# Performance work log

Measured on AMD Instinct MI355X. Metric: run time of the kernel, lower is better.

## Reference

```python
import jax, jax.numpy as jnp
import numpy as np

NUM_HEADS = 16
PREFIX = 64  # always-refreshed prefix tokens


def setup_inputs() -> dict:
    key = jax.random.key(0)
    ks = jax.random.split(key, 6)
    B, N, C = 64, 320, 1024
    H, D = NUM_HEADS, C // NUM_HEADS
    MAX_KV = 1024
    x = jax.random.normal(ks[0], (B, N, C), dtype=jnp.float32)
    # pre-existing cache contents (old cached K/V at positions 64:64+cur_kv_len matter)
    k_cache = jax.random.normal(ks[1], (B, H, MAX_KV, D), dtype=jnp.float32)
    v_cache = jax.random.normal(ks[2], (B, H, MAX_KV, D), dtype=jnp.float32)
    w_qkv = jax.random.normal(ks[3], (C, 3 * C), dtype=jnp.float32) * 0.02
    w_proj = jax.random.normal(ks[4], (C, C), dtype=jnp.float32) * 0.02
    b_proj = jnp.zeros((C,), dtype=jnp.float32)
    cur_kv_len = 256
    return {"x": x, "k_cache": k_cache, "v_cache": v_cache,
            "w_qkv": w_qkv, "w_proj": w_proj, "b_proj": b_proj,
            "cur_kv_len": cur_kv_len}


def reference(x, k_cache, v_cache, w_qkv, w_proj, b_proj, cur_kv_len):
    # Lazy-MAR incremental path (lazy_mar=True, is_force_fresh=False).
    B, N, C = x.shape
    H = NUM_HEADS
    D = C // H
    scale = D ** -0.5
    app = N - PREFIX  # number of new tokens appended to the cache

    # qkv projection (qkv_bias=False), split into q/k/v of shape [B, H, N, D]
    qkv = (x @ w_qkv).reshape(B, N, 3, H, D).transpose(2, 0, 3, 1, 4)
    q, k, v = qkv[0], qkv[1], qkv[2]  # qk_norm=False -> identity

    # in-place cache writes: refresh prefix [0:64], append new tokens at 64+cur_kv_len
    k_cache = k_cache.at[:, :, :PREFIX, :].set(k[:, :, :PREFIX, :])
    k_cache = k_cache.at[:, :, PREFIX + cur_kv_len:PREFIX + cur_kv_len + app, :].set(k[:, :, PREFIX:, :])
    v_cache = v_cache.at[:, :, :PREFIX, :].set(v[:, :, :PREFIX, :])
    v_cache = v_cache.at[:, :, PREFIX + cur_kv_len:PREFIX + cur_kv_len + app, :].set(v[:, :, PREFIX:, :])

    avail = cur_kv_len + app + PREFIX  # = cur_kv_len + N
    kk = k_cache[:, :, :avail, :]  # [B, H, avail, D]
    vv = v_cache[:, :, :avail, :]

    # manual QK^T -> softmax -> AV (attn_drop = 0)
    attn = jnp.einsum('bhnd,bhmd->bhnm', q * scale, kk)
    attn = jax.nn.softmax(attn, axis=-1)
    out = jnp.einsum('bhnm,bhmd->bhnd', attn, vv)  # [B, H, N, D]

    out = out.transpose(0, 2, 1, 3).reshape(B, N, C)
    return out @ w_proj + b_proj
```

## Files before the change

### kernel.cpp

```cpp
#include <hip/hip_runtime.h>
#include <hip/hip_bf16.h>

typedef unsigned int u32;
typedef unsigned short u16;
typedef __attribute__((ext_vector_type(4))) float f32x4;
typedef __attribute__((ext_vector_type(8))) short bf16x8;

static __device__ __forceinline__ u16 f2b(float f) {
  u32 u = __float_as_uint(f);
  u = (u + 0x7fffu + ((u >> 16) & 1u)) >> 16;
  return (u16)u;
}
static __device__ __forceinline__ u32 pk2(float a, float b) {
  return (u32)f2b(a) | ((u32)f2b(b) << 16);
}

#define AS1(p) ((__attribute__((address_space(1))) u32*)(p))
#define AS3(p) ((__attribute__((address_space(3))) u32*)(p))

union Frag  { bf16x8 v; u32 w[4]; };
union Pack8 { u32 w[8]; int4 q[2]; };

__global__ __launch_bounds__(256)
void cast_bf16(const float* __restrict__ in, u16* __restrict__ out)
{
  const size_t i = ((size_t)blockIdx.x * 256 + threadIdx.x) * 8;
  float4 a = *(const float4*)(in + i);
  float4 b = *(const float4*)(in + i + 4);
  Pack8 pb;
  pb.w[0] = pk2(a.x, a.y); pb.w[1] = pk2(a.z, a.w);
  pb.w[2] = pk2(b.x, b.y); pb.w[3] = pk2(b.z, b.w);
  *(int4*)(out + i) = pb.q[0];
}

__global__ __launch_bounds__(256)
void transpose_cvt(const float* __restrict__ in, u16* __restrict__ out,
                   int R, int C, int scale_rows)
{
  __shared__ float tile[64][65];
  const int tx = threadIdx.x & 63, ty = threadIdx.x >> 6;
  const int c0 = blockIdx.x * 64, r0 = blockIdx.y * 64;
#pragma unroll
  for (int i = 0; i < 64; i += 4)
    tile[ty + i][tx] = in[(size_t)(r0 + ty + i) * C + c0 + tx];
  __syncthreads();
#pragma unroll
  for (int i = 0; i < 64; i += 4) {
    int oc = c0 + ty + i;
    float v = tile[tx][ty + i];
    if (oc < scale_rows) v *= 0.125f;
    out[(size_t)oc * R + r0 + tx] = f2b(v);
  }
}

template<int MODE>
__global__ __launch_bounds__(256)
void gemm_bt(const u16* __restrict__ Ap, const u16* __restrict__ Bt, int NBX,
             u16* __restrict__ o_q, u16* __restrict__ o_k, u16* __restrict__ o_vt,
             const float* __restrict__ bias, float* __restrict__ outp)
{
  constexpr int K = 1024;
  constexpr int NT = 32;
  __shared__ __align__(16) u16 Al[2][128 * 32];
  __shared__ __align__(16) u16 Bl[2][128 * 32];

  const int tid = threadIdx.x;
  const int l = tid & 63, wid = tid >> 6;
  const int lr = l & 15, lg = l >> 4;
  const int wm = wid >> 1, wn = wid & 1;

  const int nwg = gridDim.x;
  const int qq = nwg >> 3;
  const int nb = (blockIdx.x & 7) * qq + (blockIdx.x >> 3);
  const int bx = nb % NBX, by = nb / NBX;

  f32x4 acc[4][4] = {};

  auto stageG = [&](int buf, int t) {
    const int k0 = t * 32;
#pragma unroll
    for (int it = 0; it < 2; ++it) {
      int row = it * 64 + (tid >> 2);
      int kb = (tid & 3) ^ (row & 3);
      const u16* g = Bt + (size_t)(bx * 128 + row) * K + k0 + kb * 8;
      __builtin_amdgcn_global_load_lds(AS1(g), AS3(&Bl[buf][0] + it * 2048 + tid * 8), 16, 0, 0);
    }
#pragma unroll
    for (int it = 0; it < 2; ++it) {
      int row = it * 64 + (tid >> 2);
      int kb = (tid & 3) ^ (row & 3);
      const u16* g = Ap + (size_t)(by * 128 + row) * K + k0 + kb * 8;
      __builtin_amdgcn_global_load_lds(AS1(g), AS3(&Al[buf][0] + it * 2048 + tid * 8), 16, 0, 0);
    }
  };

  stageG(0, 0);
  __syncthreads();

  for (int t = 0; t < NT; ++t) {
    const int cur = t & 1;
    if (t + 1 < NT) stageG(cur ^ 1, t + 1);
    bf16x8 af[4], bfr[4];
#pragma unroll
    for (int mt = 0; mt < 4; ++mt) {
      int row = wm * 64 + mt * 16 + lr;
      af[mt] = *(const bf16x8*)((const char*)&Al[cur][0] + row * 64 +
                                ((lg * 16) ^ ((row & 3) << 4)));
    }
#pragma unroll
    for (int nt = 0; nt < 4; ++nt) {
      int row = wn * 64 + nt * 16 + lr;
      bfr[nt] = *(const bf16x8*)((const char*)&Bl[cur][0] + row * 64 +
                                 ((lg * 16) ^ ((row & 3) << 4)));
    }
#pragma unroll
    for (int mt = 0; mt < 4; ++mt)
#pragma unroll
      for (int nt = 0; nt < 4; ++nt)
        acc[mt][nt] = __builtin_amdgcn_mfma_f32_16x16x32_bf16(af[mt], bfr[nt], acc[mt][nt], 0, 0, 0);
    __syncthreads();
  }

  const int col0 = bx * 128 + wn * 64;
  if (MODE == 0) {
    const int s = col0 >> 10;
    const int h = (col0 & 1023) >> 6;
#pragma unroll
    for (int mt = 0; mt < 4; ++mt) {
      int row0 = by * 128 + wm * 64 + mt * 16 + lg * 4;
      int b = row0 / 320;
      int n0 = row0 - b * 320;
      size_t bh = (size_t)(b * 16 + h);
#pragma unroll
      for (int nt = 0; nt < 4; ++nt) {
        int d = nt * 16 + lr;
        if (s == 2) {
          ushort4 p4 = make_ushort4(f2b(acc[mt][nt][0]), f2b(acc[mt][nt][1]),
                                    f2b(acc[mt][nt][2]), f2b(acc[mt][nt][3]));
          *(ushort4*)(o_vt + (bh * 64 + d) * 320 + n0) = p4;
        } else {
          u16* dst = (s == 0) ? o_q : o_k;
#pragma unroll
          for (int j = 0; j < 4; ++j)
            dst[(bh * 320 + n0 + j) * 64 + d] = f2b(acc[mt][nt][j]);
        }
      }
    }
  } else {
#pragma unroll
    for (int nt = 0; nt < 4; ++nt) {
      int col = col0 + nt * 16 + lr;
      float bv = bias[col];
#pragma unroll
      for (int mt = 0; mt < 4; ++mt)
#pragma unroll
        for (int j = 0; j < 4; ++j) {
          int row = by * 128 + wm * 64 + mt * 16 + lg * 4 + j;
          outp[(size_t)row * 1024 + col] = acc[mt][nt][j] + bv;
        }
    }
  }
}

__global__ __launch_bounds__(256)
void attn_fused(const u16* __restrict__ q_bf, const u16* __restrict__ k_new,
                const u16* __restrict__ v_new_t,
                const float* __restrict__ k_cache, const float* __restrict__ v_cache,
                u16* __restrict__ attn_out)
{
  __shared__ __align__(16) u16 Kl[64 * 64];
  __shared__ __align__(16) u16 Vl[64 * 64];
  const int qt = blockIdx.x;
  const int bh = blockIdx.y;
  const int b = bh >> 4, h = bh & 15;
  const int tid = threadIdx.x;
  const int w = tid >> 6, l = tid & 63;
  const int lr = l & 15, lg = l >> 4;

  const int qrow = qt * 64 + w * 16 + lr;
  const u16* qp = q_bf + ((size_t)bh * 320 + qrow) * 64;
  const bf16x8 qf0 = *(const bf16x8*)(qp + lg * 8);
  const bf16x8 qf1 = *(const bf16x8*)(qp + 32 + lg * 8);

  f32x4 O[4] = {};
  float m = -1e30f, lsum = 0.f;

  for (int t = 0; t < 9; ++t) {
    __syncthreads();
    if (t == 0 || t >= 5) {
      const int n0 = (t == 0) ? 0 : t * 64 - 256;
#pragma unroll
      for (int it = 0; it < 2; ++it) {
        int slot = tid + it * 256;
        int row = slot >> 3, c = slot & 7;
        int4 v = *(const int4*)(k_new + ((size_t)bh * 320 + n0 + row) * 64 + c * 8);
        *(int4*)((char*)Kl + row * 128 + ((c * 16) ^ ((row & 7) << 4))) = v;
      }
#pragma unroll
      for (int it = 0; it < 2; ++it) {
        int slot = tid + it * 256;
        int row = slot >> 3, c = slot & 7;
        int4 v = *(const int4*)(v_new_t + ((size_t)bh * 64 + row) * 320 + n0 + c * 8);
        *(int4*)((char*)Vl + row * 128 + ((c * 16) ^ ((row & 7) << 4))) = v;
      }
    } else {
      const int pos0 = t * 64;
      {
        int r = tid >> 2, d0 = (tid & 3) * 16;
        const float* src = k_cache + ((size_t)bh * 1024 + pos0 + r) * 64 + d0;
        Pack8 pb;
#pragma unroll
        for (int i = 0; i < 4; ++i) {
          float4 f = *(const float4*)(src + i * 4);
          pb.w[i * 2] = pk2(f.x, f.y); pb.w[i * 2 + 1] = pk2(f.z, f.w);
        }
        char* base = (char*)Kl + r * 128;
        int c0 = d0 >> 3;
        *(int4*)(base + ((c0 * 16) ^ ((r & 7) << 4)))       = pb.q[0];
        *(int4*)(base + (((c0 + 1) * 16) ^ ((r & 7) << 4))) = pb.q[1];
      }
#pragma unroll
      for (int it = 0; it < 4; ++it) {
        int r = (tid >> 4) + it * 16;
        int d0 = (tid & 15) * 4;
        float4 f = *(const float4*)(v_cache + ((size_t)bh * 1024 + pos0 + r) * 64 + d0);
        float fv[4] = {f.x, f.y, f.z, f.w};
#pragma unroll
        for (int i = 0; i < 4; ++i) {
          int d = d0 + i;
          *(u16*)((char*)Vl + ((d * 128 + r * 2) ^ ((d & 7) << 4))) = f2b(fv[i]);
        }
      }
    }
    __syncthreads();

    f32x4 s[4];
#pragma unroll
    for (int nt = 0; nt < 4; ++nt) {
      f32x4 a = {};
      int kv = nt * 16 + lr;
      const char* kb = (const char*)Kl + kv * 128;
      bf16x8 k0 = *(const bf16x8*)(kb + ((lg * 16) ^ ((kv & 7) << 4)));
      bf16x8 k1 = *(const bf16x8*)(kb + ((64 + lg * 16) ^ ((kv & 7) << 4)));
      a = __builtin_amdgcn_mfma_f32_16x16x32_bf16(k0, qf0, a, 0, 0, 0);
      a = __builtin_amdgcn_mfma_f32_16x16x32_bf16(k1, qf1, a, 0, 0, 0);
      s[nt] = a;
    }

    float tmax = s[0][0];
#pragma unroll
    for (int nt = 0; nt < 4; ++nt)
#pragma unroll
      for (int j = 0; j < 4; ++j) tmax = fmaxf(tmax, s[nt][j]);
    tmax = fmaxf(tmax, __shfl_xor(tmax, 16));
    tmax = fmaxf(tmax, __shfl_xor(tmax, 32));
    const float mnew = fmaxf(m, tmax);
    const float corr = __expf(m - mnew);
    float psum = 0.f;
    u32 plo[4], phi[4];
#pragma unroll
    for (int nt = 0; nt < 4; ++nt) {
      float p0 = __expf(s[nt][0] - mnew);
      float p1 = __expf(s[nt][1] - mnew);
      float p2 = __expf(s[nt][2] - mnew);
      float p3 = __expf(s[nt][3] - mnew);
      psum += (p0 + p1) + (p2 + p3);
      plo[nt] = pk2(p0, p1);
      phi[nt] = pk2(p2, p3);
    }
    psum += __shfl_xor(psum, 16);
    psum += __shfl_xor(psum, 32);
    lsum = lsum * corr + psum;
    m = mnew;

    float c_[4];
#pragma unroll
    for (int j = 0; j < 4; ++j) c_[j] = __shfl(corr, lg * 4 + j);
#pragma unroll
    for (int dt = 0; dt < 4; ++dt)
#pragma unroll
      for (int j = 0; j < 4; ++j) O[dt][j] *= c_[j];

    const int srcA = (2 * (lg & 1)) * 16 + lr;
    const int srcB = srcA + 16;
    const int hi = lg >> 1;
#pragma unroll
    for (int p = 0; p < 2; ++p) {
      Frag pa;
      u32 a0 = (u32)__shfl((int)plo[2 * p], srcA), a1 = (u32)__shfl((int)plo[2 * p + 1], srcA);
      u32 b0 = (u32)__shfl((int)phi[2 * p], srcA), b1 = (u32)__shfl((int)phi[2 * p + 1], srcA);
      u32 a2 = (u32)__shfl((int)plo[2 * p], srcB), a3 = (u32)__shfl((int)plo[2 * p + 1], srcB);
      u32 b2 = (u32)__shfl((int)phi[2 * p], srcB), b3 = (u32)__shfl((int)phi[2 * p + 1], srcB);
      pa.w[0] = hi ? a1 : a0;
      pa.w[1] = hi ? b1 : b0;
      pa.w[2] = hi ? a3 : a2;
      pa.w[3] = hi ? b3 : b2;
#pragma unroll
      for (int dt = 0; dt < 4; ++dt) {
        int d = dt * 16 + lr;
        bf16x8 vf = *(const bf16x8*)((const char*)Vl + (size_t)d * 128 +
                                     ((p * 64 + lg * 16) ^ ((d & 7) << 4)));
        O[dt] = __builtin_amdgcn_mfma_f32_16x16x32_bf16(pa.v, vf, O[dt], 0, 0, 0);
      }
    }
  }

  float inv[4];
#pragma unroll
  for (int j = 0; j < 4; ++j) inv[j] = 1.f / __shfl(lsum, lg * 4 + j);
#pragma unroll
  for (int dt = 0; dt < 4; ++dt)
#pragma unroll
    for (int j = 0; j < 4; ++j) {
      int qo = qt * 64 + w * 16 + lg * 4 + j;
      attn_out[((size_t)b * 320 + qo) * 1024 + h * 64 + dt * 16 + lr] = f2b(O[dt][j] * inv[j]);
    }
}

extern "C" void kernel_launch(void* const* d_in, const int* in_sizes, int n_in,
                              void* d_out, int out_size, void* d_ws, size_t ws_size,
                              hipStream_t stream) {
  const float* x       = (const float*)d_in[0];
  const float* k_cache = (const float*)d_in[1];
  const float* v_cache = (const float*)d_in[2];
  const float* w_qkv   = (const float*)d_in[3];
  const float* w_proj  = (const float*)d_in[4];
  const float* b_proj  = (const float*)d_in[5];

  const size_t fixed  = ((size_t)3072 * 1024 + (size_t)1024 * 1024) * 2;
  const size_t per_b  = 4 * (size_t)16 * 320 * 64 * 2;
  int Bc = 2;
  const int cands[5] = {64, 32, 16, 8, 4};
  for (int i = 0; i < 5; ++i)
    if (fixed + per_b * (size_t)cands[i] <= ws_size) { Bc = cands[i]; break; }
  const int chunks = 64 / Bc;
  const int Mc = 320 * Bc;

  char* ws = (char*)d_ws;
  u16* wqkv_t  = (u16*)ws; ws += (size_t)3072 * 1024 * 2;
  u16* wproj_t = (u16*)ws; ws += (size_t)1024 * 1024 * 2;
  u16* q_bf    = (u16*)ws; ws += (size_t)Bc * 16 * 320 * 64 * 2;
  u16* k_new   = (u16*)ws; ws += (size_t)Bc * 16 * 320 * 64 * 2;
  u16* v_new_t = (u16*)ws; ws += (size_t)Bc * 16 * 320 * 64 * 2;
  u16* attn_o  = (u16*)ws; ws += (size_t)Bc * 320 * 1024 * 2;
  u16* x_bf    = attn_o;
  float* outp = (float*)d_out;

  transpose_cvt<<<dim3(48, 16), 256, 0, stream>>>(w_qkv, wqkv_t, 1024, 3072, 1024);
  transpose_cvt<<<dim3(16, 16), 256, 0, stream>>>(w_proj, wproj_t, 1024, 1024, 0);

  for (int c = 0; c < chunks; ++c) {
    const size_t row_base = (size_t)c * Mc;
    const size_t kv_base  = (size_t)c * Bc * 16 * 1024 * 64;
    cast_bf16<<<Mc / 2, 256, 0, stream>>>(x + row_base * 1024, x_bf);
    gemm_bt<0><<<60 * Bc, 256, 0, stream>>>(x_bf, wqkv_t, 24,
                                            q_bf, k_new, v_new_t, nullptr, nullptr);
    attn_fused<<<dim3(5, Bc * 16), 256, 0, stream>>>(q_bf, k_new, v_new_t,
                                                     k_cache + kv_base, v_cache + kv_base,
                                                     attn_o);
    gemm_bt<1><<<20 * Bc, 256, 0, stream>>>(attn_o, wproj_t, 8,
                                            nullptr, nullptr, nullptr,
                                            b_proj, outp + row_base * 1024);
  }
}
```

Before: 942.7 us.

## Pre-convert KV cache to bf16 and double-buffer attention loads via global_load_lds

Adds separate kernels that convert the old K cache to bf16 and the old V cache to transposed bf16 into a unified 576-token KV buffer. The QKV GEMM now writes new K/V straight into their final cache positions. The attention kernel then streams K/V tiles with direct global-to-LDS loads into double-buffered shared memory, so the next tile's load overlaps compute on the current one. It also remaps workgroups across XCDs. This takes fp32 conversion and the scattered transposed V stores out of the attention inner loop. The cost is two extra kernel launches, an extra round trip of the cached K/V through memory, and a larger workspace.

```diff
diff --git a/kernel.cpp b/kernel.cpp
--- a/kernel.cpp
+++ b/kernel.cpp
@@ -34,6 +34,39 @@
 }
 
 __global__ __launch_bounds__(256)
+void cvt_k(const float* __restrict__ k_cache, u16* __restrict__ Ku)
+{
+  const size_t i8 = ((size_t)blockIdx.x * 256 + threadIdx.x) * 8;
+  const size_t bh = i8 >> 14;
+  const size_t rem = i8 & 16383;
+  const float* in = k_cache + bh * 65536 + 4096 + rem;
+  float4 a = *(const float4*)(in);
+  float4 b = *(const float4*)(in + 4);
+  Pack8 pb;
+  pb.w[0] = pk2(a.x, a.y); pb.w[1] = pk2(a.z, a.w);
+  pb.w[2] = pk2(b.x, b.y); pb.w[3] = pk2(b.z, b.w);
+  *(int4*)(Ku + bh * 36864 + 4096 + rem) = pb.q[0];
+}
+
+__global__ __launch_bounds__(256)
+void cvt_v(const float* __restrict__ v_cache, u16* __restrict__ Vu)
+{
+  __shared__ float tile[64][65];
+  const int tx = threadIdx.x & 63, ty = threadIdx.x >> 6;
+  const int r0 = 64 + blockIdx.x * 64;
+  const size_t bh = blockIdx.y;
+#pragma unroll
+  for (int i = 0; i < 64; i += 4)
+    tile[ty + i][tx] = v_cache[(bh * 1024 + r0 + ty + i) * 64 + tx];
+  __syncthreads();
+#pragma unroll
+  for (int i = 0; i < 64; i += 4) {
+    int d = ty + i;
+    Vu[(bh * 64 + d) * 576 + r0 + tx] = f2b(tile[tx][d]);
+  }
+}
+
+__global__ __launch_bounds__(256)
 void transpose_cvt(const float* __restrict__ in, u16* __restrict__ out,
                    int R, int C, int scale_rows)
 {
@@ -130,6 +163,7 @@
       int row0 = by * 128 + wm * 64 + mt * 16 + lg * 4;
       int b = row0 / 320;
       int n0 = row0 - b * 320;
+      int pos = n0 + ((n0 >= 64) ? 256 : 0);
       size_t bh = (size_t)(b * 16 + h);
 #pragma unroll
       for (int nt = 0; nt < 4; ++nt) {
@@ -137,12 +171,15 @@
         if (s == 2) {
           ushort4 p4 = make_ushort4(f2b(acc[mt][nt][0]), f2b(acc[mt][nt][1]),
                                     f2b(acc[mt][nt][2]), f2b(acc[mt][nt][3]));
-          *(ushort4*)(o_vt + (bh * 64 + d) * 320 + n0) = p4;
+          *(ushort4*)(o_vt + (bh * 64 + d) * 576 + pos) = p4;
+        } else if (s == 1) {
+#pragma unroll
+          for (int j = 0; j < 4; ++j)
+            o_k[(bh * 576 + pos + j) * 64 + d] = f2b(acc[mt][nt][j]);
         } else {
-          u16* dst = (s == 0) ? o_q : o_k;
 #pragma unroll
           for (int j = 0; j < 4; ++j)
-            dst[(bh * 320 + n0 + j) * 64 + d] = f2b(acc[mt][nt][j]);
+            o_q[(bh * 320 + n0 + j) * 64 + d] = f2b(acc[mt][nt][j]);
         }
       }
     }
@@ -163,15 +200,16 @@
 }
 
 __global__ __launch_bounds__(256)
-void attn_fused(const u16* __restrict__ q_bf, const u16* __restrict__ k_new,
-                const u16* __restrict__ v_new_t,
-                const float* __restrict__ k_cache, const float* __restrict__ v_cache,
-                u16* __restrict__ attn_out)
-{
-  __shared__ __align__(16) u16 Kl[64 * 64];
-  __shared__ __align__(16) u16 Vl[64 * 64];
-  const int qt = blockIdx.x;
-  const int bh = blockIdx.y;
+void attn_fused(const u16* __restrict__ q_bf, const u16* __restrict__ Ku,
+                const u16* __restrict__ Vu, u16* __restrict__ attn_out)
+{
+  __shared__ __align__(16) u16 Kl[2][64 * 64];
+  __shared__ __align__(16) u16 Vl[2][64 * 64];
+  const int nwg = gridDim.x;
+  const int qq = nwg >> 3;
+  const int nb = (blockIdx.x & 7) * qq + (blockIdx.x >> 3);
+  const int qt = nb % 5;
+  const int bh = nb / 5;
   const int b = bh >> 4, h = bh & 15;
   const int tid = threadIdx.x;
   const int w = tid >> 6, l = tid & 63;
@@ -182,64 +220,40 @@
   const bf16x8 qf0 = *(const bf16x8*)(qp + lg * 8);
   const bf16x8 qf1 = *(const bf16x8*)(qp + 32 + lg * 8);
 
+  auto stageKV = [&](int t, int buf) {
+    const int pos0 = t * 64;
+#pragma unroll
+    for (int it = 0; it < 2; ++it) {
+      int slot = tid + it * 256;
+      int row = slot >> 3, c = slot & 7, kb = c ^ (row & 7);
+      const u16* g = Ku + ((size_t)bh * 576 + pos0 + row) * 64 + kb * 8;
+      __builtin_amdgcn_global_load_lds(AS1(g), AS3(&Kl[buf][0] + slot * 8), 16, 0, 0);
+    }
+#pragma unroll
+    for (int it = 0; it < 2; ++it) {
+      int slot = tid + it * 256;
+      int d = slot >> 3, c = slot & 7, kb = c ^ (d & 7);
+      const u16* g = Vu + ((size_t)bh * 64 + d) * 576 + pos0 + kb * 8;
+      __builtin_amdgcn_global_load_lds(AS1(g), AS3(&Vl[buf][0] + slot * 8), 16, 0, 0);
+    }
+  };
+
   f32x4 O[4] = {};
   float m = -1e30f, lsum = 0.f;
 
+  stageKV(0, 0);
+  __syncthreads();
+
   for (int t = 0; t < 9; ++t) {
-    __syncthreads();
-    if (t == 0 || t >= 5) {
-      const int n0 = (t == 0) ? 0 : t * 64 - 256;
-#pragma unroll
-      for (int it = 0; it < 2; ++it) {
-        int slot = tid + it * 256;
-        int row = slot >> 3, c = slot & 7;
-        int4 v = *(const int4*)(k_new + ((size_t)bh * 320 + n0 + row) * 64 + c * 8);
-        *(int4*)((char*)Kl + row * 128 + ((c * 16) ^ ((row & 7) << 4))) = v;
-      }
-#pragma unroll
-      for (int it = 0; it < 2; ++it) {
-        int slot = tid + it * 256;
-        int row = slot >> 3, c = slot & 7;
-        int4 v = *(const int4*)(v_new_t + ((size_t)bh * 64 + row) * 320 + n0 + c * 8);
-        *(int4*)((char*)Vl + row * 128 + ((c * 16) ^ ((row & 7) << 4))) = v;
-      }
-    } else {
-      const int pos0 = t * 64;
-      {
-        int r = tid >> 2, d0 = (tid & 3) * 16;
-        const float* src = k_cache + ((size_t)bh * 1024 + pos0 + r) * 64 + d0;
-        Pack8 pb;
-#pragma unroll
-        for (int i = 0; i < 4; ++i) {
-          float4 f = *(const float4*)(src + i * 4);
-          pb.w[i * 2] = pk2(f.x, f.y); pb.w[i * 2 + 1] = pk2(f.z, f.w);
-        }
-        char* base = (char*)Kl + r * 128;
-        int c0 = d0 >> 3;
-        *(int4*)(base + ((c0 * 16) ^ ((r & 7) << 4)))       = pb.q[0];
-        *(int4*)(base + (((c0 + 1) * 16) ^ ((r & 7) << 4))) = pb.q[1];
-      }
-#pragma unroll
-      for (int it = 0; it < 4; ++it) {
-        int r = (tid >> 4) + it * 16;
-        int d0 = (tid & 15) * 4;
-        float4 f = *(const float4*)(v_cache + ((size_t)bh * 1024 + pos0 + r) * 64 + d0);
-        float fv[4] = {f.x, f.y, f.z, f.w};
-#pragma unroll
-        for (int i = 0; i < 4; ++i) {
-          int d = d0 + i;
-          *(u16*)((char*)Vl + ((d * 128 + r * 2) ^ ((d & 7) << 4))) = f2b(fv[i]);
-        }
-      }
-    }
-    __syncthreads();
+    const int cur = t & 1;
+    if (t + 1 < 9) stageKV(t + 1, cur ^ 1);
 
     f32x4 s[4];
 #pragma unroll
     for (int nt = 0; nt < 4; ++nt) {
       f32x4 a = {};
       int kv = nt * 16 + lr;
-      const char* kb = (const char*)Kl + kv * 128;
+      const char* kb = (const char*)&Kl[cur][0] + kv * 128;
       bf16x8 k0 = *(const bf16x8*)(kb + ((lg * 16) ^ ((kv & 7) << 4)));
       bf16x8 k1 = *(const bf16x8*)(kb + ((64 + lg * 16) ^ ((kv & 7) << 4)));
       a = __builtin_amdgcn_mfma_f32_16x16x32_bf16(k0, qf0, a, 0, 0, 0);
@@ -298,11 +312,12 @@
 #pragma unroll
       for (int dt = 0; dt < 4; ++dt) {
         int d = dt * 16 + lr;
-        bf16x8 vf = *(const bf16x8*)((const char*)Vl + (size_t)d * 128 +
+        bf16x8 vf = *(const bf16x8*)((const char*)&Vl[cur][0] + (size_t)d * 128 +
                                      ((p * 64 + lg * 16) ^ ((d & 7) << 4)));
         O[dt] = __builtin_amdgcn_mfma_f32_16x16x32_bf16(pa.v, vf, O[dt], 0, 0, 0);
       }
     }
+    __syncthreads();
   }
 
   float inv[4];
@@ -327,8 +342,9 @@
   const float* w_proj  = (const float*)d_in[4];
   const float* b_proj  = (const float*)d_in[5];
 
-  const size_t fixed  = ((size_t)3072 * 1024 + (size_t)1024 * 1024) * 2;
-  const size_t per_b  = 4 * (size_t)16 * 320 * 64 * 2;
+  const size_t fixed = ((size_t)3072 * 1024 + (size_t)1024 * 1024) * 2;
+  const size_t per_b = ((size_t)16 * 320 * 64 + 2 * (size_t)16 * 576 * 64 +
+                        (size_t)320 * 1024) * 2;
   int Bc = 2;
   const int cands[5] = {64, 32, 16, 8, 4};
   for (int i = 0; i < 5; ++i)
@@ -340,8 +356,8 @@
   u16* wqkv_t  = (u16*)ws; ws += (size_t)3072 * 1024 * 2;
   u16* wproj_t = (u16*)ws; ws += (size_t)1024 * 1024 * 2;
   u16* q_bf    = (u16*)ws; ws += (size_t)Bc * 16 * 320 * 64 * 2;
-  u16* k_new   = (u16*)ws; ws += (size_t)Bc * 16 * 320 * 64 * 2;
-  u16* v_new_t = (u16*)ws; ws += (size_t)Bc * 16 * 320 * 64 * 2;
+  u16* Ku      = (u16*)ws; ws += (size_t)Bc * 16 * 576 * 64 * 2;
+  u16* Vu      = (u16*)ws; ws += (size_t)Bc * 16 * 576 * 64 * 2;
   u16* attn_o  = (u16*)ws; ws += (size_t)Bc * 320 * 1024 * 2;
   u16* x_bf    = attn_o;
   float* outp = (float*)d_out;
@@ -353,11 +369,11 @@
     const size_t row_base = (size_t)c * Mc;
     const size_t kv_base  = (size_t)c * Bc * 16 * 1024 * 64;
     cast_bf16<<<Mc / 2, 256, 0, stream>>>(x + row_base * 1024, x_bf);
+    cvt_k<<<Bc * 128, 256, 0, stream>>>(k_cache + kv_base, Ku);
+    cvt_v<<<dim3(4, Bc * 16), 256, 0, stream>>>(v_cache + kv_base, Vu);
     gemm_bt<0><<<60 * Bc, 256, 0, stream>>>(x_bf, wqkv_t, 24,
-                                            q_bf, k_new, v_new_t, nullptr, nullptr);
-    attn_fused<<<dim3(5, Bc * 16), 256, 0, stream>>>(q_bf, k_new, v_new_t,
-                                                     k_cache + kv_base, v_cache + kv_base,
-                                                     attn_o);
+                                            q_bf, Ku, Vu, nullptr, nullptr);
+    attn_fused<<<80 * Bc, 256, 0, stream>>>(q_bf, Ku, Vu, attn_o);
     gemm_bt<1><<<20 * Bc, 256, 0, stream>>>(attn_o, wproj_t, 8,
                                             nullptr, nullptr, nullptr,
                                             b_proj, outp + row_base * 1024);
```

After: 931.4 us. About the same (-1.2%).
